# Kernel optimization log

Measured on AMD Instinct MI355X. Metric: run time of the kernel, lower is better.

The kernel has to match this reference:

```python
import jax, jax.numpy as jnp
import numpy as np

SHAPE = (64, 64, 64)
N0 = 4000
K = 5  # subm conv kernel size -> 125 taps


def _neighbors(coors, shp):
    # coors: [N,4] int (b,z,y,x), batch=1. Returns [N,125] int32 neighbor row ids, -1 if absent.
    offs = np.stack(np.meshgrid(np.arange(-2, 3), np.arange(-2, 3), np.arange(-2, 3), indexing='ij'), -1).reshape(-1, 3)
    shp = np.asarray(shp)
    grid = -np.ones(tuple(shp), np.int32)
    grid[coors[:, 1], coors[:, 2], coors[:, 3]] = np.arange(len(coors), dtype=np.int32)
    nb = coors[:, None, 1:4] + offs[None]  # [N,125,3]
    valid = ((nb >= 0) & (nb < shp)).all(-1)
    nbc = np.clip(nb, 0, shp - 1)
    nbr = grid[nbc[..., 0], nbc[..., 1], nbc[..., 2]]
    return np.where(valid, nbr, -1).astype(np.int32)


def _pool_map(coors, shp):
    # kernel 2 stride 2 sparse max pool: parent cell = spatial // 2
    out_shp = [s // 2 for s in shp]
    sp = coors[:, 1:4] // 2
    lin = (sp[:, 0] * out_shp[1] + sp[:, 1]) * out_shp[2] + sp[:, 2]
    uniq, inv = np.unique(lin, return_inverse=True)
    z = uniq // (out_shp[1] * out_shp[2])
    r = uniq % (out_shp[1] * out_shp[2])
    nc = np.stack([np.zeros_like(z), z, r // out_shp[2], r % out_shp[2]], 1).astype(np.int32)
    return inv.astype(np.int32), nc, out_shp


_PAIRS = [(3, 64), (64, 64), (64, 96), (96, 96), (96, 128), (128, 128), (128, 160), (160, 160), (160, 192), (192, 192), (192, 224), (224, 224), (224, 256), (256, 256)]
_WNAMES = ['w0a', 'w0b', 'w1a', 'w1b', 'w2a', 'w2b', 'w3a', 'w3b', 'w4a', 'w4b', 'w5a', 'w5b', 'w6a', 'w6b']


def setup_inputs() -> dict:
    rng = np.random.RandomState(0)
    lin = rng.choice(SHAPE[0] * SHAPE[1] * SHAPE[2], N0, replace=False)
    z = lin // (SHAPE[1] * SHAPE[2])
    r = lin % (SHAPE[1] * SHAPE[2])
    coors = np.stack([np.zeros_like(z), z, r // SHAPE[2], r % SHAPE[2]], 1).astype(np.int32)
    inp = {}
    c, shp = coors, list(SHAPE)
    for l in range(7):
        inp['nbr%d' % l] = jnp.asarray(_neighbors(c, shp))
        if l < 6:
            pm, c, shp = _pool_map(c, shp)
            inp['pool%d' % l] = jnp.asarray(pm)
    key = jax.random.key(0)
    for name, (ci, co) in zip(_WNAMES, _PAIRS):
        key, k = jax.random.split(key)
        inp[name] = jax.random.normal(k, (K ** 3, ci, co), jnp.float32) * (K ** 3 * ci) ** -0.5
    key, kf = jax.random.split(key)
    inp['features'] = jax.random.normal(kf, (N0, 3), jnp.float32)
    inp['coors'] = jnp.asarray(coors)
    inp['batch_size'] = 1
    return inp


def _subm(feats, nbr, w):
    # gather-GEMM-scatter form of SubMConv3d (bias=False): out active set == in active set
    valid = nbr >= 0  # [N,125]
    g = jnp.take(feats, jnp.maximum(nbr, 0), axis=0)  # [N,125,Cin]
    g = jnp.where(valid[:, :, None], g, jnp.zeros((), feats.dtype))
    return jnp.einsum('nkc,kco->no', g, w)  # [N,Cout]


def reference(features, coors, batch_size, nbr0, nbr1, nbr2, nbr3, nbr4, nbr5, nbr6, pool0, pool1, pool2, pool3, pool4, pool5, w0a, w0b, w1a, w1b, w2a, w2b, w3a, w3b, w4a, w4b, w5a, w5b, w6a, w6b):
    nbrs = (nbr0, nbr1, nbr2, nbr3, nbr4, nbr5, nbr6)
    pools = (pool0, pool1, pool2, pool3, pool4, pool5)
    ws = ((w0a, w0b), (w1a, w1b), (w2a, w2b), (w3a, w3b), (w4a, w4b), (w5a, w5b), (w6a, w6b))
    x = features
    for l in range(7):
        x = _subm(x, nbrs[l], ws[l][0])
        x = _subm(x, nbrs[l], ws[l][1])
        if l < 6:
            # sparse max pool over active voxels of each 2x2x2 cell
            x = jax.ops.segment_max(x, pools[l], num_segments=nbrs[l + 1].shape[0])
    return x
```

## Files before the change

kernel.cpp:

```cpp
#include <hip/hip_runtime.h>
#include <stddef.h>
#include <stdint.h>

#define KTAPS 125

typedef _Float16 f16x8 __attribute__((ext_vector_type(8)));
typedef _Float16 f16x4 __attribute__((ext_vector_type(4)));
typedef float    f32x4 __attribute__((ext_vector_type(4)));

template<int NT, int KRC>
__global__ __launch_bounds__(256) void subm_mfma(
    const _Float16* __restrict__ finh, const int* __restrict__ nbr,
    const _Float16* __restrict__ wt, _Float16* __restrict__ Pout,
    int N, int CinP, int TS, int CS)
{
    constexpr int BN = NT * 32;
    const int tid  = threadIdx.x;
    const int lane = tid & 63;
    const int wid  = tid >> 6;
    const int wy   = wid & 1;
    const int wx   = wid >> 1;
    const int r15  = lane & 15;
    const int g4   = lane >> 4;

    int rowtile, ts, cs;
    if (KRC == 8) {
        int L = blockIdx.x, q = L >> 3;
        int TSo = TS >> 3;
        ts = (L & 7) + 8 * (q % TSo);
        rowtile = q / TSo;
        cs = 0;
    } else {
        rowtile = 0; ts = blockIdx.y; cs = blockIdx.z;
    }

    const int row0 = rowtile * 64;
    const int k0   = (ts * KTAPS) / TS;
    const int k1   = ((ts + 1) * KTAPS) / TS;
    const int KR   = k1 - k0;
    const int CC   = CinP >> 5;
    const int cc0  = (cs * CC) / CS;
    const int cc1  = ((cs + 1) * CC) / CS;

    int nb0[KRC], nb1[KRC];
    unsigned m0[KRC], m1[KRC];
    #pragma unroll
    for (int j = 0; j < KRC; ++j) {
        int v0 = -1, v1 = -1;
        if (j < KR) {
            int r0 = row0 + wy * 32 + r15;
            int r1 = r0 + 16;
            if (r0 < N) v0 = nbr[(size_t)r0 * KTAPS + k0 + j];
            if (r1 < N) v1 = nbr[(size_t)r1 * KTAPS + k0 + j];
        }
        nb0[j] = (v0 < 0) ? N : v0;
        nb1[j] = (v1 < 0) ? N : v1;
        m0[j] = (unsigned)(__ballot(v0 >= 0) & 0xFFFFull);
        m1[j] = (unsigned)(__ballot(v1 >= 0) & 0xFFFFull);
    }

    f32x4 acc[2][NT];
    #pragma unroll
    for (int mt = 0; mt < 2; ++mt)
        #pragma unroll
        for (int nf = 0; nf < NT; ++nf)
            acc[mt][nf] = (f32x4){0.f, 0.f, 0.f, 0.f};

    const size_t wchunk = (size_t)32 * BN;
    const int    boffh  = (g4 * BN + wx * (NT * 16) + r15) * 8;

    for (int cc = cc0; cc < cc1; ++cc) {
        #pragma unroll
        for (int j = 0; j < KRC; ++j) {
            unsigned mm0 = m0[j], mm1 = m1[j];
            if (!(mm0 | mm1)) continue;
            f16x8 a0 = {}, a1 = {};
            if (mm0) a0 = *(const f16x8*)(finh + (size_t)nb0[j] * CinP + cc * 32 + g4 * 8);
            if (mm1) a1 = *(const f16x8*)(finh + (size_t)nb1[j] * CinP + cc * 32 + g4 * 8);
            const _Float16* base = wt + ((size_t)(k0 + j) * CC + cc) * wchunk + boffh;
            #pragma unroll
            for (int nf = 0; nf < NT; ++nf) {
                f16x8 b = *(const f16x8*)(base + (size_t)nf * 128);
                if (mm0) acc[0][nf] = __builtin_amdgcn_mfma_f32_16x16x32_f16(a0, b, acc[0][nf], 0, 0, 0);
                if (mm1) acc[1][nf] = __builtin_amdgcn_mfma_f32_16x16x32_f16(a1, b, acc[1][nf], 0, 0, 0);
            }
        }
    }

    _Float16* base = Pout + (size_t)(ts * CS + cs) * ((size_t)N * BN);
    #pragma unroll
    for (int mt = 0; mt < 2; ++mt) {
        #pragma unroll
        for (int q = 0; q < 4; ++q) {
            int r = row0 + wy * 32 + mt * 16 + g4 * 4 + q;
            if (r < N) {
                #pragma unroll
                for (int nf = 0; nf < NT; ++nf)
                    base[(size_t)r * BN + wx * (NT * 16) + nf * 16 + r15] =
                        (_Float16)acc[mt][nf][q];
            }
        }
    }
}

__global__ __launch_bounds__(256) void reduce_a(
    const _Float16* __restrict__ P, _Float16* __restrict__ H,
    int N, int BN, int S, float scale)
{
    const int qi = threadIdx.x & 15;
    const int st = threadIdx.x >> 4;
    const int q  = blockIdx.x * 16 + qi;
    const size_t i4  = (size_t)q * 4;
    const size_t tot = (size_t)N * BN;
    f32x4 s = (f32x4){0.f, 0.f, 0.f, 0.f};
    if (i4 < tot) {
        for (int si = st; si < S; si += 16) {
            f16x4 p = *(const f16x4*)&P[(size_t)si * tot + i4];
            s[0] += (float)p[0]; s[1] += (float)p[1];
            s[2] += (float)p[2]; s[3] += (float)p[3];
        }
    }
    __shared__ f32x4 red[16][16];
    red[st][qi] = s;
    __syncthreads();
    #pragma unroll
    for (int off = 8; off > 0; off >>= 1) {
        if (st < off) red[st][qi] += red[st + off][qi];
        __syncthreads();
    }
    if (st == 0 && i4 < (size_t)(N + 1) * BN) {
        f32x4 r = red[0][qi];
        f16x4 h;
        h[0] = (_Float16)(r[0] * scale); h[1] = (_Float16)(r[1] * scale);
        h[2] = (_Float16)(r[2] * scale); h[3] = (_Float16)(r[3] * scale);
        *(f16x4*)&H[i4] = h;
    }
}

__device__ __forceinline__ unsigned enc_f32(float f) {
    unsigned u = __float_as_uint(f);
    return (u & 0x80000000u) ? ~u : (u | 0x80000000u);
}

__global__ __launch_bounds__(256) void reduce_b(
    const _Float16* __restrict__ P, const int* __restrict__ pm,
    unsigned* __restrict__ ENC, float* __restrict__ dout,
    int N, int BN, int S, float fscale, int isLast)
{
    const int qi = threadIdx.x & 15;
    const int st = threadIdx.x >> 4;
    const int q  = blockIdx.x * 16 + qi;
    const size_t i4  = (size_t)q * 4;
    const size_t tot = (size_t)N * BN;
    f32x4 s = (f32x4){0.f, 0.f, 0.f, 0.f};
    if (i4 < tot) {
        for (int si = st; si < S; si += 16) {
            f16x4 p = *(const f16x4*)&P[(size_t)si * tot + i4];
            s[0] += (float)p[0]; s[1] += (float)p[1];
            s[2] += (float)p[2]; s[3] += (float)p[3];
        }
    }
    __shared__ f32x4 red[16][16];
    red[st][qi] = s;
    __syncthreads();
    #pragma unroll
    for (int off = 8; off > 0; off >>= 1) {
        if (st < off) red[st][qi] += red[st + off][qi];
        __syncthreads();
    }
    if (st == 0 && i4 < tot) {
        f32x4 r = red[0][qi];
        if (isLast) {
            dout[i4 + 0] = r[0] * fscale; dout[i4 + 1] = r[1] * fscale;
            dout[i4 + 2] = r[2] * fscale; dout[i4 + 3] = r[3] * fscale;
        } else {
            int row = (int)(i4 / BN), c = (int)(i4 % BN);
            unsigned* e = &ENC[(size_t)pm[row] * BN + c];
            atomicMax(e + 0, enc_f32(r[0]));
            atomicMax(e + 1, enc_f32(r[1]));
            atomicMax(e + 2, enc_f32(r[2]));
            atomicMax(e + 3, enc_f32(r[3]));
        }
    }
}

__global__ __launch_bounds__(256) void pool_dec(
    unsigned* __restrict__ ENC, _Float16* __restrict__ H, int Nout, int C, float scale)
{
    int i = blockIdx.x * 256 + threadIdx.x;
    if (i < Nout * C) {
        unsigned u = ENC[i];
        float f = __uint_as_float((u & 0x80000000u) ? (u ^ 0x80000000u) : ~u);
        H[i] = (_Float16)(f * scale);
        ENC[i] = 0u;
    } else if (i < (Nout + 1) * C) {
        H[i] = (_Float16)0.f;
    }
}

__global__ __launch_bounds__(256) void tap_flags(
    const int* n0, const int* n1, const int* n2, const int* n3,
    const int* n4, const int* n5, const int* n6,
    int N0, int N1, int N2, int N3, int N4, int N5, int N6,
    unsigned* __restrict__ flags)
{
    int l = blockIdx.y, k = blockIdx.x;
    const int* nb; int N;
    switch (l) {
        case 0: nb = n0; N = N0; break;  case 1: nb = n1; N = N1; break;
        case 2: nb = n2; N = N2; break;  case 3: nb = n3; N = N3; break;
        case 4: nb = n4; N = N4; break;  case 5: nb = n5; N = N5; break;
        default: nb = n6; N = N6; break;
    }
    bool any = false;
    for (int r = threadIdx.x; r < N; r += 256) any |= (nb[(size_t)r * KTAPS + k] >= 0);
    bool a = __syncthreads_or(any);
    if (threadIdx.x == 0) flags[l * KTAPS + k] = a ? 1u : 0u;
}

__global__ __launch_bounds__(256) void cvt_weights(
    const float* __restrict__ wa, const float* __restrict__ wb,
    _Float16* __restrict__ ta, _Float16* __restrict__ tb,
    const unsigned* __restrict__ flags,
    int CinA, int CCa, int CoutA, int splitA,
    int CinB, int CCb, int CoutB)
{
    int k = blockIdx.x;
    if (!flags[k]) return;
    int by = blockIdx.y;
    const float* w; _Float16* t; int Cin, CC, Cout, cc, c0;
    if (by < splitA) { w = wa; t = ta; Cin = CinA; CC = CCa; Cout = CoutA;
                       cc = by / (CoutA / 32); c0 = (by % (CoutA / 32)) * 32; }
    else { by -= splitA; w = wb; t = tb; Cin = CinB; CC = CCb; Cout = CoutB;
           cc = by / (CoutB / 32); c0 = (by % (CoutB / 32)) * 32; }

    __shared__ float T[32][33];
    int tid = threadIdx.x;
    #pragma unroll
    for (int p = 0; p < 4; ++p) {
        int e = tid + p * 256;
        int r = e >> 5, cl = e & 31;
        int ci = cc * 32 + r;
        T[r][cl] = (ci < Cin) ? w[((size_t)k * Cin + ci) * Cout + c0 + cl] : 0.f;
    }
    __syncthreads();
    if (tid < 128) {
        int g = tid >> 5, co = tid & 31;
        f16x8 h;
        #pragma unroll
        for (int j = 0; j < 8; ++j) h[j] = (_Float16)T[g * 8 + j][co];
        *(f16x8*)&t[((size_t)k * CC + cc) * (32 * (size_t)Cout) + ((size_t)g * Cout + c0 + co) * 8] = h;
    }
}

__global__ __launch_bounds__(256) void init_all(
    const float* __restrict__ feat, _Float16* __restrict__ H,
    unsigned* __restrict__ ENC, int N0, int nE)
{
    int i = blockIdx.x * 256 + threadIdx.x;
    if (i < nE) ENC[i] = 0u;
    int nH = (N0 + 1) * 32;
    if (i < nH) {
        int r = i >> 5, cl = i & 31;
        H[i] = (r < N0 && cl < 3) ? (_Float16)feat[r * 3 + cl] : (_Float16)0.f;
    }
}

static inline int pick_ts(int rt)
{
    int ts = (1536 / rt) & ~7;
    if (ts < 16) ts = 16;
    if (ts > 120) ts = 120;
    return ts;
}

static void conv_dispatch(int NT, int krc8, dim3 g, hipStream_t s, const _Float16* fin,
                          const int* nbr, const _Float16* wt, _Float16* P,
                          int N, int CinP, int TS, int CS)
{
    if (krc8) {
        switch (NT) {
            case 2: subm_mfma<2,8><<<g,256,0,s>>>(fin,nbr,wt,P,N,CinP,TS,CS); break;
            case 3: subm_mfma<3,8><<<g,256,0,s>>>(fin,nbr,wt,P,N,CinP,TS,CS); break;
            case 4: subm_mfma<4,8><<<g,256,0,s>>>(fin,nbr,wt,P,N,CinP,TS,CS); break;
            case 5: subm_mfma<5,8><<<g,256,0,s>>>(fin,nbr,wt,P,N,CinP,TS,CS); break;
            case 6: subm_mfma<6,8><<<g,256,0,s>>>(fin,nbr,wt,P,N,CinP,TS,CS); break;
            case 7: subm_mfma<7,8><<<g,256,0,s>>>(fin,nbr,wt,P,N,CinP,TS,CS); break;
            case 8: subm_mfma<8,8><<<g,256,0,s>>>(fin,nbr,wt,P,N,CinP,TS,CS); break;
        }
    } else {
        switch (NT) {
            case 2: subm_mfma<2,1><<<g,256,0,s>>>(fin,nbr,wt,P,N,CinP,TS,CS); break;
            case 3: subm_mfma<3,1><<<g,256,0,s>>>(fin,nbr,wt,P,N,CinP,TS,CS); break;
            case 4: subm_mfma<4,1><<<g,256,0,s>>>(fin,nbr,wt,P,N,CinP,TS,CS); break;
            case 5: subm_mfma<5,1><<<g,256,0,s>>>(fin,nbr,wt,P,N,CinP,TS,CS); break;
            case 6: subm_mfma<6,1><<<g,256,0,s>>>(fin,nbr,wt,P,N,CinP,TS,CS); break;
            case 7: subm_mfma<7,1><<<g,256,0,s>>>(fin,nbr,wt,P,N,CinP,TS,CS); break;
            case 8: subm_mfma<8,1><<<g,256,0,s>>>(fin,nbr,wt,P,N,CinP,TS,CS); break;
        }
    }
}

extern "C" void kernel_launch(void* const* d_in, const int* in_sizes, int n_in,
                              void* d_out, int out_size, void* d_ws, size_t ws_size,
                              hipStream_t stream)
{
    const int* nbr[7]; const int* pm[6]; int Ns[7];
    {
        int idx = 0;
        for (int l = 0; l < 7; ++l) {
            nbr[l] = (const int*)d_in[idx];
            Ns[l]  = in_sizes[idx] / KTAPS;
            ++idx;
            if (l < 6) { pm[l] = (const int*)d_in[idx]; ++idx; }
        }
    }
    const float* w[14];
    for (int i = 0; i < 14; ++i) w[i] = (const float*)d_in[13 + i];
    const float* feat = (const float*)d_in[27];

    static const int CI[14]  = {3,64, 64,96, 96,128, 128,160, 160,192, 192,224, 224,256};
    static const int CO[14]  = {64,64, 96,96, 128,128, 160,160, 192,192, 224,224, 256,256};
    static const int KSH[14] = {0,3, 2,2, 1,1, 0,0, 0,1, 0,2, 2,3};
    const float finalScale = 1.0f / 131072.0f;
    int CinP[14];
    for (int i = 0; i < 14; ++i) CinP[i] = (CI[i] < 32) ? 32 : CI[i];

    int TSv[14], CSv[14], K8v[14];
    size_t maxP = 0, maxHa = 0, maxHb = 0, maxE = 0, maxWA = 0, maxWB = 0;
    for (int l = 0; l < 7; ++l) {
        int rt = (Ns[l] + 63) / 64;
        for (int q = 0; q < 2; ++q) {
            int i = 2 * l + q;
            if (rt > 1) { TSv[i] = pick_ts(rt); CSv[i] = 1; K8v[i] = 1; }
            else        { TSv[i] = KTAPS; CSv[i] = CinP[i] / 32; K8v[i] = 0; }
            size_t p = (size_t)TSv[i] * CSv[i] * Ns[l] * CO[i];
            if (p > maxP) maxP = p;
        }
        size_t ha = (size_t)(Ns[l] + 1) * CinP[2*l];   if (ha > maxHa) maxHa = ha;
        size_t hb = (size_t)(Ns[l] + 1) * CinP[2*l+1]; if (hb > maxHb) maxHb = hb;
        if (l < 6) { size_t e = (size_t)Ns[l+1] * CO[2*l+1]; if (e > maxE) maxE = e; }
        size_t wa = (size_t)KTAPS * CinP[2*l] * CO[2*l];     if (wa > maxWA) maxWA = wa;
        size_t wb = (size_t)KTAPS * CinP[2*l+1] * CO[2*l+1]; if (wb > maxWB) maxWB = wb;
    }
    size_t off = 0;
    auto carve = [&](size_t bytes) -> void* {
        void* p = (char*)d_ws + off;
        off = (off + bytes + 255) & ~(size_t)255;
        return p;
    };
    _Float16*  P    = (_Float16*)carve(maxP * 2);
    _Float16*  Ha   = (_Float16*)carve(maxHa * 2);
    _Float16*  Hb   = (_Float16*)carve(maxHb * 2);
    unsigned*  ENC  = (unsigned*)carve(maxE * 4);
    _Float16*  wtA  = (_Float16*)carve(maxWA * 2);
    _Float16*  wtB  = (_Float16*)carve(maxWB * 2);
    unsigned*  flags= (unsigned*)carve(7 * KTAPS * 4);

    {
        int nMax = (int)maxE;
        int nH = (Ns[0] + 1) * 32;
        if (nH > nMax) nMax = nH;
        init_all<<<(nMax + 255) / 256, 256, 0, stream>>>(feat, Ha, ENC, Ns[0], (int)maxE);
    }
    tap_flags<<<dim3(KTAPS, 7), 256, 0, stream>>>(
        nbr[0], nbr[1], nbr[2], nbr[3], nbr[4], nbr[5], nbr[6],
        Ns[0], Ns[1], Ns[2], Ns[3], Ns[4], Ns[5], Ns[6], flags);

    for (int l = 0; l < 7; ++l) {
        int ia = 2 * l, ib = 2 * l + 1;
        int N = Ns[l];
        int rt = (N + 63) / 64;
        int splitA = (CinP[ia] / 32) * (CO[ia] / 32);
        int splitB = (CinP[ib] / 32) * (CO[ib] / 32);
        cvt_weights<<<dim3(KTAPS, splitA + splitB), 256, 0, stream>>>(
            w[ia], w[ib], wtA, wtB, flags + l * KTAPS,
            CI[ia], CinP[ia] / 32, CO[ia], splitA,
            CI[ib], CinP[ib] / 32, CO[ib]);

        {
            int TS = TSv[ia], CS = CSv[ia], BN = CO[ia];
            dim3 g = K8v[ia] ? dim3(rt * TS) : dim3(1, TS, CS);
            conv_dispatch(BN / 32, K8v[ia], g, stream, Ha, nbr[l], wtA, P, N, CinP[ia], TS, CS);
            int quads = ((N + 1) * BN) / 4;
            reduce_a<<<(quads + 15) / 16, 256, 0, stream>>>(P, Hb, N, BN, TS * CS,
                                                            (float)(1 << KSH[ib]));
        }
        {
            int TS = TSv[ib], CS = CSv[ib], BN = CO[ib];
            dim3 g = K8v[ib] ? dim3(rt * TS) : dim3(1, TS, CS);
            conv_dispatch(BN / 32, K8v[ib], g, stream, Hb, nbr[l], wtB, P, N, CinP[ib], TS, CS);
            int quads = (N * BN) / 4;
            reduce_b<<<(quads + 15) / 16, 256, 0, stream>>>(
                P, (l < 6) ? pm[l] : nullptr, ENC, (float*)d_out,
                N, BN, TS * CS, finalScale, (l == 6) ? 1 : 0);
        }
        if (l < 6) {
            int C = CO[ib], Nout = Ns[l + 1];
            int tot2 = (Nout + 1) * C;
            pool_dec<<<(tot2 + 255) / 256, 256, 0, stream>>>(ENC, Ha, Nout, C,
                                                             (float)(1 << KSH[2 * l + 2]));
        }
    }
}
```

Baseline: 479.7 us.

## Software-pipeline gather and weight loads ahead of MFMA in subm conv

Restructures the inner tap loop into a double-buffered register pipeline: the next tap's neighbor features and weight fragments are loaded while the current tap's MFMAs run. Per-half-wave masks are replaced by a single wave-uniform skip flag, so loads are issued unconditionally (absent neighbors are redirected to row N) and only whole empty taps are skipped. This aims to hide global load latency, at the cost of more registers and redundant loads for taps that end up skipped. A leftover duplicate assignment of the mask remains in the code.

```diff
diff --git a/kernel.cpp b/kernel.cpp
--- a/kernel.cpp
+++ b/kernel.cpp
@@ -43,7 +43,7 @@
     const int cc1  = ((cs + 1) * CC) / CS;
 
     int nb0[KRC], nb1[KRC];
-    unsigned m0[KRC], m1[KRC];
+    unsigned mj[KRC];
     #pragma unroll
     for (int j = 0; j < KRC; ++j) {
         int v0 = -1, v1 = -1;
@@ -55,8 +55,9 @@
         }
         nb0[j] = (v0 < 0) ? N : v0;
         nb1[j] = (v1 < 0) ? N : v1;
-        m0[j] = (unsigned)(__ballot(v0 >= 0) & 0xFFFFull);
-        m1[j] = (unsigned)(__ballot(v1 >= 0) & 0xFFFFull);
+        mj[j] = (unsigned)(__ballot((v0 | v1) >= 0 ? 1 : 0) & 0xFFFFFFFFull) |
+                (unsigned)(__ballot((v0 | v1) >= 0 ? 1 : 0) >> 32);
+        mj[j] = (__ballot(v0 >= 0) | __ballot(v1 >= 0)) ? 1u : 0u;
     }
 
     f32x4 acc[2][NT];
@@ -69,20 +70,73 @@
     const size_t wchunk = (size_t)32 * BN;
     const int    boffh  = (g4 * BN + wx * (NT * 16) + r15) * 8;
 
-    for (int cc = cc0; cc < cc1; ++cc) {
-        #pragma unroll
-        for (int j = 0; j < KRC; ++j) {
-            unsigned mm0 = m0[j], mm1 = m1[j];
-            if (!(mm0 | mm1)) continue;
-            f16x8 a0 = {}, a1 = {};
-            if (mm0) a0 = *(const f16x8*)(finh + (size_t)nb0[j] * CinP + cc * 32 + g4 * 8);
-            if (mm1) a1 = *(const f16x8*)(finh + (size_t)nb1[j] * CinP + cc * 32 + g4 * 8);
+    if (KRC == 8) {
+        f16x8 A0[2], B0[NT], A1[2], B1[NT];
+
+        auto LA = [&](f16x8 (&a)[2], int j, int cc) {
+            a[0] = *(const f16x8*)(finh + (size_t)nb0[j] * CinP + cc * 32 + g4 * 8);
+            a[1] = *(const f16x8*)(finh + (size_t)nb1[j] * CinP + cc * 32 + g4 * 8);
+        };
+        auto LB = [&](f16x8 (&b)[NT], int j, int cc) {
             const _Float16* base = wt + ((size_t)(k0 + j) * CC + cc) * wchunk + boffh;
             #pragma unroll
+            for (int nf = 0; nf < NT; ++nf)
+                b[nf] = *(const f16x8*)(base + (size_t)nf * 128);
+        };
+        auto FM = [&](f16x8 (&a)[2], f16x8 (&b)[NT]) {
+            #pragma unroll
             for (int nf = 0; nf < NT; ++nf) {
-                f16x8 b = *(const f16x8*)(base + (size_t)nf * 128);
-                if (mm0) acc[0][nf] = __builtin_amdgcn_mfma_f32_16x16x32_f16(a0, b, acc[0][nf], 0, 0, 0);
-                if (mm1) acc[1][nf] = __builtin_amdgcn_mfma_f32_16x16x32_f16(a1, b, acc[1][nf], 0, 0, 0);
+                acc[0][nf] = __builtin_amdgcn_mfma_f32_16x16x32_f16(a[0], b[nf], acc[0][nf], 0, 0, 0);
+                acc[1][nf] = __builtin_amdgcn_mfma_f32_16x16x32_f16(a[1], b[nf], acc[1][nf], 0, 0, 0);
+            }
+        };
+
+        LA(A0, 0, cc0); LB(B0, 0, cc0);
+        for (int cc = cc0; cc < cc1; ++cc) {
+            int ncc = (cc + 1 < cc1) ? cc + 1 : cc0;
+            #pragma unroll
+            for (int j = 0; j < KRC; j += 2) {
+                LA(A1, j + 1, cc); LB(B1, j + 1, cc);
+                if (mj[j]) FM(A0, B0);
+                if (j + 2 < KRC) { LA(A0, j + 2, cc); LB(B0, j + 2, cc); }
+                else             { LA(A0, 0, ncc);    LB(B0, 0, ncc);    }
+                if (mj[j + 1]) FM(A1, B1);
+            }
+        }
+    } else {
+        f16x8 A0[2], B0[NT], A1[2], B1[NT];
+        auto LAc = [&](f16x8 (&a)[2], int cc) {
+            a[0] = *(const f16x8*)(finh + (size_t)nb0[0] * CinP + cc * 32 + g4 * 8);
+            a[1] = *(const f16x8*)(finh + (size_t)nb1[0] * CinP + cc * 32 + g4 * 8);
+        };
+        auto LBc = [&](f16x8 (&b)[NT], int cc) {
+            const _Float16* base = wt + ((size_t)k0 * CC + cc) * wchunk + boffh;
+            #pragma unroll
+            for (int nf = 0; nf < NT; ++nf)
+                b[nf] = *(const f16x8*)(base + (size_t)nf * 128);
+        };
+        auto FMc = [&](f16x8 (&a)[2], f16x8 (&b)[NT]) {
+            #pragma unroll
+            for (int nf = 0; nf < NT; ++nf) {
+                acc[0][nf] = __builtin_amdgcn_mfma_f32_16x16x32_f16(a[0], b[nf], acc[0][nf], 0, 0, 0);
+                acc[1][nf] = __builtin_amdgcn_mfma_f32_16x16x32_f16(a[1], b[nf], acc[1][nf], 0, 0, 0);
+            }
+        };
+        if (mj[0]) {
+            LAc(A0, cc0); LBc(B0, cc0);
+            int cc = cc0;
+            while (true) {
+                int n1 = cc + 1;
+                bool h1 = n1 < cc1;
+                if (h1) { LAc(A1, n1); LBc(B1, n1); }
+                FMc(A0, B0);
+                if (!h1) break;
+                int n2 = n1 + 1;
+                bool h2 = n2 < cc1;
+                if (h2) { LAc(A0, n2); LBc(B0, n2); }
+                FMc(A1, B1);
+                if (!h2) break;
+                cc = n2;
             }
         }
     }
```

New measurement: 529.9 us. 1.1x slower.
